# Kernel optimization log

Hardware: AMD Instinct MI355X
Metric: run time of the kernel (lower is better)

The kernel has to match this reference:

```python
import jax, jax.numpy as jnp
import numpy as np

NUM_HEADS = 8
HEAD_DIM = 64  # hidden_size 512 / 8 heads


def setup_inputs() -> dict:
    key = jax.random.key(0)
    ks = jax.random.split(key, 9)
    B, S, D, H = 64, 512, 512, 512  # batch, feat_num, input_size, hidden_size
    s = 0.02
    return {
        "x": jax.random.normal(ks[0], (B, S, D), dtype=jnp.float32),
        "wq": jax.random.normal(ks[1], (D, H), dtype=jnp.float32) * s,
        "bq": jax.random.normal(ks[2], (H,), dtype=jnp.float32) * s,
        "wk": jax.random.normal(ks[3], (D, H), dtype=jnp.float32) * s,
        "bk": jax.random.normal(ks[4], (H,), dtype=jnp.float32) * s,
        "wv": jax.random.normal(ks[5], (D, H), dtype=jnp.float32) * s,
        "bv": jax.random.normal(ks[6], (H,), dtype=jnp.float32) * s,
        "wo": jax.random.normal(ks[7], (H, D), dtype=jnp.float32) * s,
        "bo": jax.random.normal(ks[8], (D,), dtype=jnp.float32) * s,
    }


def reference(x, wq, bq, wk, bk, wv, bv, wo, bo):
    B, S, D = x.shape
    # QKV projections -> [B, heads, S, head_dim]
    def split_heads(t):
        return t.reshape(B, S, NUM_HEADS, HEAD_DIM).transpose(0, 2, 1, 3)
    q = split_heads(x @ wq + bq)
    k = split_heads(x @ wk + bk)
    v = split_heads(x @ wv + bv)
    # attention: [B, h, S, S]
    scores = jnp.einsum("bhsd,bhtd->bhst", q, k) / jnp.sqrt(
        jnp.asarray(HEAD_DIM, dtype=x.dtype)
    )
    probs = jax.nn.softmax(scores, axis=-1)  # dropout p=0 -> identity
    ctx = jnp.einsum("bhst,bhtd->bhsd", probs, v)
    ctx = ctx.transpose(0, 2, 1, 3).reshape(B, S, NUM_HEADS * HEAD_DIM)
    # output dense + residual + relu (dropout identity)
    out = jax.nn.relu(x + (ctx @ wo + bo))
    return out
```

## Files before the change

kernel.cpp:

```cpp
#include <hip/hip_runtime.h>
#include <hip/hip_bf16.h>

typedef unsigned short u16;
typedef unsigned int u32;
typedef __attribute__((ext_vector_type(8))) short short8;
typedef __attribute__((ext_vector_type(4))) float f32x4;
typedef __attribute__((ext_vector_type(4))) _Float16 f16x4;

static __device__ __forceinline__ u16 f2b(float f) {
  unsigned u = __builtin_bit_cast(unsigned, f);
  unsigned r = u + 0x7fffu + ((u >> 16) & 1u);
  return (u16)(r >> 16);
}
static __device__ __forceinline__ unsigned pk2(float a, float b) {
  return (unsigned)f2b(a) | ((unsigned)f2b(b) << 16);
}
static __device__ __forceinline__ u32 pkh(float a, float b) {
  return __builtin_bit_cast(u32, __builtin_amdgcn_cvt_pkrtz(a, b));
}

static __device__ __forceinline__ void gl_lds16(const u16* g, u16* l) {
  __builtin_amdgcn_global_load_lds(
      (const __attribute__((address_space(1))) unsigned*)g,
      (__attribute__((address_space(3))) unsigned*)l, 16, 0, 0);
}


__global__ __launch_bounds__(256) void prep(
    const float* __restrict__ wq, const float* __restrict__ wk,
    const float* __restrict__ wv, const float* __restrict__ wo,
    const float* __restrict__ x, u16* __restrict__ wqkv_t,
    u16* __restrict__ wo_t, u16* __restrict__ xb) {
  int t = blockIdx.x * 256 + threadIdx.x;
  if (t < 786432) {
    int n = t >> 9, k = t & 511;
    const float* w = (n < 512) ? wq : (n < 1024 ? wk : wv);
    wqkv_t[(size_t)n * 512 + k] = f2b(w[k * 512 + (n & 511)]);
  } else if (t < 1048576) {
    int j = t - 786432;
    int n = j >> 9, k = j & 511;
    wo_t[(size_t)n * 512 + k] = f2b(wo[k * 512 + n]);
  } else {
    size_t i = (size_t)(t - 1048576) * 4;
    float4 v = *reinterpret_cast<const float4*>(&x[i]);
    uint2 p;
    p.x = pk2(v.x, v.y);
    p.y = pk2(v.z, v.w);
    *reinterpret_cast<uint2*>(&xb[i]) = p;
  }
}

__global__ __launch_bounds__(256, 4) void gemm_qkv(
    const u16* __restrict__ xb, const u16* __restrict__ wt,
    const float* __restrict__ bq, const float* __restrict__ bk,
    const float* __restrict__ bv, u16* __restrict__ qkv) {
  __shared__ u16 As[128 * 64];
  __shared__ u16 Bs[128 * 64];
  const int tid = threadIdx.x;
  const int wave = tid >> 6, lane = tid & 63;
  const int wm = wave & 1, wn = wave >> 1;
  const int lr = lane & 15, lg = lane >> 4;
  const int n0 = blockIdx.x * 128, m0 = blockIdx.y * 128;

  const f32x4 fz = {0.f, 0.f, 0.f, 0.f};
  f32x4 acc[4][4];
#pragma unroll
  for (int i = 0; i < 4; ++i)
#pragma unroll
    for (int j = 0; j < 4; ++j) acc[i][j] = fz;

  for (int kb = 0; kb < 512; kb += 64) {
#pragma unroll
    for (int j = 0; j < 4; ++j) {
      const int cb = (wave * 4 + j) * 64;
      const int c = cb + lane;
      const int r = c >> 3;
      const int cg = (c & 7) ^ (r & 7);
      gl_lds16(&xb[(size_t)(m0 + r) * 512 + kb + (cg << 3)], &As[cb * 8]);
      gl_lds16(&wt[(size_t)(n0 + r) * 512 + kb + (cg << 3)], &Bs[cb * 8]);
    }
    __syncthreads();
#pragma unroll
    for (int ks = 0; ks < 2; ++ks) {
      short8 af[4], bb[4];
#pragma unroll
      for (int i = 0; i < 4; ++i)
        af[i] = *reinterpret_cast<const short8*>(
            &As[(wm * 64 + i * 16 + lr) * 64 +
                (((ks * 4 + lg) ^ (lr & 7)) << 3)]);
#pragma unroll
      for (int j = 0; j < 4; ++j)
        bb[j] = *reinterpret_cast<const short8*>(
            &Bs[(wn * 64 + j * 16 + lr) * 64 +
                (((ks * 4 + lg) ^ (lr & 7)) << 3)]);
#pragma unroll
      for (int i = 0; i < 4; ++i)
#pragma unroll
        for (int j = 0; j < 4; ++j)
          acc[i][j] = __builtin_amdgcn_mfma_f32_16x16x32_bf16(
              af[i], bb[j], acc[i][j], 0, 0, 0);
    }
    __syncthreads();
  }
#pragma unroll
  for (int i = 0; i < 4; ++i) {
    const int row0 = m0 + wm * 64 + i * 16 + lg * 4;
#pragma unroll
    for (int j = 0; j < 4; ++j) {
      const int col = n0 + wn * 64 + j * 16 + lr;
      const float bias =
          (col < 512) ? bq[col] : (col < 1024 ? bk[col - 512] : bv[col - 1024]);
#pragma unroll
      for (int r = 0; r < 4; ++r) {
        float v = acc[i][j][r] + bias;
        u16 ov;
        if (col < 512)
          ov = f2b(v * 0.125f);
        else if (col < 1024)
          ov = f2b(v);
        else
          ov = __builtin_bit_cast(u16, (_Float16)v);
        qkv[(size_t)(row0 + r) * 1536 + col] = ov;
      }
    }
  }
}

__global__ __launch_bounds__(256, 3) void attn(const u16* __restrict__ qkv,
                                               u16* __restrict__ ctx) {
  __shared__ u16 QOs[128 * 66];
  __shared__ u16 Ks[2][64 * 64];
  __shared__ u16 VsT[2][64 * 70];

  const int tid = threadIdx.x;
  const int wave = tid >> 6, lane = tid & 63;
  const int lr = lane & 15, lg = lane >> 4;
  const int bx = blockIdx.x;
  const int q0 = (bx & 3) * 128;
  const int h = (bx >> 2) & 7;
  const int b = bx >> 5;
  const size_t rowbase = (size_t)b * 512;

#pragma unroll
  for (int j = 0; j < 4; ++j) {
    const int cb = (wave * 4 + j) * 64, c = cb + lane;
    const int r = c >> 3, cg = (c & 7) ^ (r & 7);
    gl_lds16(&qkv[(rowbase + q0 + r) * 1536 + h * 64 + (cg << 3)],
             &QOs[cb * 8]);
  }
#pragma unroll
  for (int j = 0; j < 2; ++j) {
    const int cb = (wave * 2 + j) * 64, c = cb + lane;
    const int r = c >> 3, cg = (c & 7) ^ (r & 7);
    gl_lds16(&qkv[(rowbase + r) * 1536 + 512 + h * 64 + (cg << 3)],
             &Ks[0][cb * 8]);
  }
  uint4 vreg[2];
#pragma unroll
  for (int i = 0; i < 2; ++i) {
    int idx = tid + i * 256, r = idx >> 3, cg = idx & 7;
    vreg[i] = *reinterpret_cast<const uint4*>(
        &qkv[(rowbase + r) * 1536 + 1024 + h * 64 + cg * 8]);
  }
#pragma unroll
  for (int i = 0; i < 2; ++i) {
    int idx = tid + i * 256, r = idx >> 3, cg = idx & 7;
    const u16* pv = reinterpret_cast<const u16*>(&vreg[i]);
#pragma unroll
    for (int jj = 0; jj < 8; ++jj) VsT[0][(cg * 8 + jj) * 70 + r] = pv[jj];
  }
  __syncthreads();

  short8 aq[2][2];
#pragma unroll
  for (int g = 0; g < 2; ++g)
#pragma unroll
    for (int ks = 0; ks < 2; ++ks)
      aq[g][ks] = *reinterpret_cast<const short8*>(
          &QOs[(wave * 32 + g * 16 + lr) * 64 +
               (((ks * 4 + lg) ^ (lr & 7)) << 3)]);

  const f32x4 fz = {0.f, 0.f, 0.f, 0.f};
  f32x4 oacc[2][4];
#pragma unroll
  for (int g = 0; g < 2; ++g)
#pragma unroll
    for (int dt = 0; dt < 4; ++dt) oacc[g][dt] = fz;
  float lsum[2] = {0.f, 0.f};

  for (int tt = 0; tt < 8; ++tt) {
    const int buf = tt & 1;
    if (tt < 7) {
#pragma unroll
      for (int j = 0; j < 2; ++j) {
        const int cb = (wave * 2 + j) * 64, c = cb + lane;
        const int r = c >> 3, cg = (c & 7) ^ (r & 7);
        gl_lds16(&qkv[(rowbase + (tt + 1) * 64 + r) * 1536 + 512 + h * 64 +
                      (cg << 3)],
                 &Ks[buf ^ 1][cb * 8]);
      }
#pragma unroll
      for (int i = 0; i < 2; ++i) {
        int idx = tid + i * 256, r = idx >> 3, cg = idx & 7;
        vreg[i] = *reinterpret_cast<const uint4*>(
            &qkv[(rowbase + (tt + 1) * 64 + r) * 1536 + 1024 + h * 64 + cg * 8]);
      }
    }

    f32x4 st[2][4];
#pragma unroll
    for (int g = 0; g < 2; ++g)
#pragma unroll
      for (int mt = 0; mt < 4; ++mt) st[g][mt] = fz;
#pragma unroll
    for (int mt = 0; mt < 4; ++mt) {
      short8 k0 = *reinterpret_cast<const short8*>(
          &Ks[buf][(mt * 16 + lr) * 64 + ((lg ^ (lr & 7)) << 3)]);
      short8 k1 = *reinterpret_cast<const short8*>(
          &Ks[buf][(mt * 16 + lr) * 64 + (((4 + lg) ^ (lr & 7)) << 3)]);
#pragma unroll
      for (int g = 0; g < 2; ++g) {
        st[g][mt] = __builtin_amdgcn_mfma_f32_16x16x32_bf16(k0, aq[g][0],
                                                            st[g][mt], 0, 0, 0);
        st[g][mt] = __builtin_amdgcn_mfma_f32_16x16x32_bf16(k1, aq[g][1],
                                                            st[g][mt], 0, 0, 0);
      }
    }

    f16x4 pfrag[2][4];
#pragma unroll
    for (int g = 0; g < 2; ++g)
#pragma unroll
      for (int mt = 0; mt < 4; ++mt) {
        float e0 = __expf(st[g][mt][0]), e1 = __expf(st[g][mt][1]);
        float e2 = __expf(st[g][mt][2]), e3 = __expf(st[g][mt][3]);
        lsum[g] += (e0 + e1) + (e2 + e3);
        uint2 uu;
        uu.x = pkh(e0, e1);
        uu.y = pkh(e2, e3);
        pfrag[g][mt] = __builtin_bit_cast(f16x4, uu);
      }

#pragma unroll
    for (int dt = 0; dt < 4; ++dt) {
#pragma unroll
      for (int tw = 0; tw < 4; ++tw) {
        const int a0 = (dt * 16 + lr) * 70 + tw * 16 + lg * 4;
        uint2 uu;
        uu.x = *reinterpret_cast<const u32*>(&VsT[buf][a0]);
        uu.y = *reinterpret_cast<const u32*>(&VsT[buf][a0 + 2]);
        f16x4 vf = __builtin_bit_cast(f16x4, uu);
#pragma unroll
        for (int g = 0; g < 2; ++g)
          oacc[g][dt] = __builtin_amdgcn_mfma_f32_16x16x16f16(
              vf, pfrag[g][tw], oacc[g][dt], 0, 0, 0);
      }
    }

    if (tt < 7) {
#pragma unroll
      for (int i = 0; i < 2; ++i) {
        int idx = tid + i * 256, r = idx >> 3, cg = idx & 7;
        const u16* pv = reinterpret_cast<const u16*>(&vreg[i]);
#pragma unroll
        for (int jj = 0; jj < 8; ++jj)
          VsT[buf ^ 1][(cg * 8 + jj) * 70 + r] = pv[jj];
      }
    }
    __syncthreads();
  }

#pragma unroll
  for (int g = 0; g < 2; ++g) {
    float s = lsum[g];
    s += __shfl_xor(s, 16);
    s += __shfl_xor(s, 32);
    lsum[g] = 1.0f / s;
  }
#pragma unroll
  for (int g = 0; g < 2; ++g)
#pragma unroll
    for (int dt = 0; dt < 4; ++dt) {
      f32x4 o = oacc[g][dt];
      const float li = lsum[g];
      const int base = (wave * 32 + g * 16 + lr) * 66 + dt * 16 + lg * 4;
      *reinterpret_cast<u32*>(&QOs[base]) = pk2(o[0] * li, o[1] * li);
      *reinterpret_cast<u32*>(&QOs[base + 2]) = pk2(o[2] * li, o[3] * li);
    }
  __syncthreads();
  const size_t coff = (rowbase + q0) * 512 + h * 64;
#pragma unroll
  for (int i = 0; i < 4; ++i) {
    int idx = tid + i * 256, r = idx >> 3, cg = idx & 7;
    const u16* src = &QOs[r * 66 + cg * 8];
    uint4 w;
    w.x = *reinterpret_cast<const u32*>(&src[0]);
    w.y = *reinterpret_cast<const u32*>(&src[2]);
    w.z = *reinterpret_cast<const u32*>(&src[4]);
    w.w = *reinterpret_cast<const u32*>(&src[6]);
    *reinterpret_cast<uint4*>(&ctx[coff + (size_t)r * 512 + cg * 8]) = w;
  }
}

__global__ __launch_bounds__(256, 4) void gemm_out(
    const u16* __restrict__ ctx, const u16* __restrict__ wot,
    const float* __restrict__ x, const float* __restrict__ bo,
    float* __restrict__ out) {
  __shared__ u16 As[128 * 64];
  __shared__ u16 Bs[128 * 64];
  const int tid = threadIdx.x;
  const int wave = tid >> 6, lane = tid & 63;
  const int wm = wave & 1, wn = wave >> 1;
  const int lr = lane & 15, lg = lane >> 4;
  const int n0 = blockIdx.x * 128, m0 = blockIdx.y * 128;

  const f32x4 fz = {0.f, 0.f, 0.f, 0.f};
  f32x4 acc[4][4];
#pragma unroll
  for (int i = 0; i < 4; ++i)
#pragma unroll
    for (int j = 0; j < 4; ++j) acc[i][j] = fz;

  for (int kb = 0; kb < 512; kb += 64) {
#pragma unroll
    for (int j = 0; j < 4; ++j) {
      const int cb = (wave * 4 + j) * 64;
      const int c = cb + lane;
      const int r = c >> 3;
      const int cg = (c & 7) ^ (r & 7);
      gl_lds16(&ctx[(size_t)(m0 + r) * 512 + kb + (cg << 3)], &As[cb * 8]);
      gl_lds16(&wot[(size_t)(n0 + r) * 512 + kb + (cg << 3)], &Bs[cb * 8]);
    }
    __syncthreads();
#pragma unroll
    for (int ks = 0; ks < 2; ++ks) {
      short8 af[4], bb[4];
#pragma unroll
      for (int i = 0; i < 4; ++i)
        af[i] = *reinterpret_cast<const short8*>(
            &As[(wm * 64 + i * 16 + lr) * 64 +
                (((ks * 4 + lg) ^ (lr & 7)) << 3)]);
#pragma unroll
      for (int j = 0; j < 4; ++j)
        bb[j] = *reinterpret_cast<const short8*>(
            &Bs[(wn * 64 + j * 16 + lr) * 64 +
                (((ks * 4 + lg) ^ (lr & 7)) << 3)]);
#pragma unroll
      for (int i = 0; i < 4; ++i)
#pragma unroll
        for (int j = 0; j < 4; ++j)
          acc[i][j] = __builtin_amdgcn_mfma_f32_16x16x32_bf16(
              af[i], bb[j], acc[i][j], 0, 0, 0);
    }
    __syncthreads();
  }
#pragma unroll
  for (int i = 0; i < 4; ++i) {
#pragma unroll
    for (int j = 0; j < 4; ++j) {
      const int col = n0 + wn * 64 + j * 16 + lr;
#pragma unroll
      for (int r = 0; r < 4; ++r) {
        const int row = m0 + wm * 64 + i * 16 + lg * 4 + r;
        float v = acc[i][j][r] + bo[col] + x[(size_t)row * 512 + col];
        out[(size_t)row * 512 + col] = fmaxf(v, 0.0f);
      }
    }
  }
}

extern "C" void kernel_launch(void* const* d_in, const int* in_sizes, int n_in,
                              void* d_out, int out_size, void* d_ws,
                              size_t ws_size, hipStream_t stream) {
  const float* x = (const float*)d_in[0];
  const float* wq = (const float*)d_in[1];
  const float* bq = (const float*)d_in[2];
  const float* wk = (const float*)d_in[3];
  const float* bk = (const float*)d_in[4];
  const float* wv = (const float*)d_in[5];
  const float* bv = (const float*)d_in[6];
  const float* wo = (const float*)d_in[7];
  const float* bo = (const float*)d_in[8];
  float* out = (float*)d_out;

  char* ws = (char*)d_ws;
  u16* qkv = (u16*)ws;
  u16* ctx = (u16*)(ws + 100663296);
  u16* xb = ctx;
  u16* wqkv_t = (u16*)(ws + 134217728);
  u16* wo_t = (u16*)(ws + 135790592);

  hipLaunchKernelGGL(prep, dim3(20480), dim3(256), 0, stream, wq, wk, wv, wo,
                     x, wqkv_t, wo_t, xb);
  hipLaunchKernelGGL(gemm_qkv, dim3(12, 256), dim3(256), 0, stream, xb, wqkv_t,
                     bq, bk, bv, qkv);
  hipLaunchKernelGGL(attn, dim3(2048), dim3(256), 0, stream, qkv, ctx);
  hipLaunchKernelGGL(gemm_out, dim3(4, 256), dim3(256), 0, stream, ctx, wo_t,
                     x, bo, out);
}
```

Baseline: 307.3 us.

## Remap block indices per XCD, write ctx in place, read bf16 residual

Block indices in the QKV GEMM, attention and output GEMM are remapped so consecutive blocks on the same XCD share rows and heads, aiming for better L2 reuse. Attention writes its context output into the Q slot of the qkv buffer, and the output GEMM reads it with a 1536 stride, removing the separate ctx buffer. The residual is read from the bf16 copy of x instead of fp32 to halve those bytes. This adds rounding error to the residual path.

```diff
diff --git a/kernel.cpp b/kernel.cpp
--- a/kernel.cpp
+++ b/kernel.cpp
@@ -11,6 +11,9 @@
   unsigned u = __builtin_bit_cast(unsigned, f);
   unsigned r = u + 0x7fffu + ((u >> 16) & 1u);
   return (u16)(r >> 16);
+}
+static __device__ __forceinline__ float b2f(u16 v) {
+  return __builtin_bit_cast(float, (u32)v << 16);
 }
 static __device__ __forceinline__ unsigned pk2(float a, float b) {
   return (unsigned)f2b(a) | ((unsigned)f2b(b) << 16);
@@ -60,7 +63,10 @@
   const int wave = tid >> 6, lane = tid & 63;
   const int wm = wave & 1, wn = wave >> 1;
   const int lr = lane & 15, lg = lane >> 4;
-  const int n0 = blockIdx.x * 128, m0 = blockIdx.y * 128;
+  const int id = blockIdx.x;
+  const int xcd = id & 7, s = id >> 3;
+  const int n0 = (s % 12) * 128;
+  const int m0 = ((s / 12) * 8 + xcd) * 128;
 
   const f32x4 fz = {0.f, 0.f, 0.f, 0.f};
   f32x4 acc[4][4];
@@ -126,8 +132,7 @@
   }
 }
 
-__global__ __launch_bounds__(256, 3) void attn(const u16* __restrict__ qkv,
-                                               u16* __restrict__ ctx) {
+__global__ __launch_bounds__(256, 3) void attn(u16* __restrict__ qkv) {
   __shared__ u16 QOs[128 * 66];
   __shared__ u16 Ks[2][64 * 64];
   __shared__ u16 VsT[2][64 * 70];
@@ -136,9 +141,10 @@
   const int wave = tid >> 6, lane = tid & 63;
   const int lr = lane & 15, lg = lane >> 4;
   const int bx = blockIdx.x;
-  const int q0 = (bx & 3) * 128;
-  const int h = (bx >> 2) & 7;
-  const int b = bx >> 5;
+  const int xcd = bx & 7, s = bx >> 3;
+  const int q0 = (s & 3) * 128;
+  const int bh = (s >> 2) * 8 + xcd;
+  const int b = bh >> 3, h = bh & 7;
   const size_t rowbase = (size_t)b * 512;
 
 #pragma unroll
@@ -272,10 +278,10 @@
 
 #pragma unroll
   for (int g = 0; g < 2; ++g) {
-    float s = lsum[g];
-    s += __shfl_xor(s, 16);
-    s += __shfl_xor(s, 32);
-    lsum[g] = 1.0f / s;
+    float s2 = lsum[g];
+    s2 += __shfl_xor(s2, 16);
+    s2 += __shfl_xor(s2, 32);
+    lsum[g] = 1.0f / s2;
   }
 #pragma unroll
   for (int g = 0; g < 2; ++g)
@@ -288,7 +294,6 @@
       *reinterpret_cast<u32*>(&QOs[base + 2]) = pk2(o[2] * li, o[3] * li);
     }
   __syncthreads();
-  const size_t coff = (rowbase + q0) * 512 + h * 64;
 #pragma unroll
   for (int i = 0; i < 4; ++i) {
     int idx = tid + i * 256, r = idx >> 3, cg = idx & 7;
@@ -298,13 +303,14 @@
     w.y = *reinterpret_cast<const u32*>(&src[2]);
     w.z = *reinterpret_cast<const u32*>(&src[4]);
     w.w = *reinterpret_cast<const u32*>(&src[6]);
-    *reinterpret_cast<uint4*>(&ctx[coff + (size_t)r * 512 + cg * 8]) = w;
+    *reinterpret_cast<uint4*>(
+        &qkv[(rowbase + q0 + r) * 1536 + h * 64 + cg * 8]) = w;
   }
 }
 
 __global__ __launch_bounds__(256, 4) void gemm_out(
-    const u16* __restrict__ ctx, const u16* __restrict__ wot,
-    const float* __restrict__ x, const float* __restrict__ bo,
+    const u16* __restrict__ ctxq, const u16* __restrict__ wot,
+    const u16* __restrict__ xb, const float* __restrict__ bo,
     float* __restrict__ out) {
   __shared__ u16 As[128 * 64];
   __shared__ u16 Bs[128 * 64];
@@ -312,7 +318,10 @@
   const int wave = tid >> 6, lane = tid & 63;
   const int wm = wave & 1, wn = wave >> 1;
   const int lr = lane & 15, lg = lane >> 4;
-  const int n0 = blockIdx.x * 128, m0 = blockIdx.y * 128;
+  const int id = blockIdx.x;
+  const int xcd = id & 7, s = id >> 3;
+  const int n0 = (s & 3) * 128;
+  const int m0 = ((s >> 2) * 8 + xcd) * 128;
 
   const f32x4 fz = {0.f, 0.f, 0.f, 0.f};
   f32x4 acc[4][4];
@@ -328,7 +337,7 @@
       const int c = cb + lane;
       const int r = c >> 3;
       const int cg = (c & 7) ^ (r & 7);
-      gl_lds16(&ctx[(size_t)(m0 + r) * 512 + kb + (cg << 3)], &As[cb * 8]);
+      gl_lds16(&ctxq[(size_t)(m0 + r) * 1536 + kb + (cg << 3)], &As[cb * 8]);
       gl_lds16(&wot[(size_t)(n0 + r) * 512 + kb + (cg << 3)], &Bs[cb * 8]);
     }
     __syncthreads();
@@ -362,7 +371,7 @@
 #pragma unroll
       for (int r = 0; r < 4; ++r) {
         const int row = m0 + wm * 64 + i * 16 + lg * 4 + r;
-        float v = acc[i][j][r] + bo[col] + x[(size_t)row * 512 + col];
+        float v = acc[i][j][r] + bo[col] + b2f(xb[(size_t)row * 512 + col]);
         out[(size_t)row * 512 + col] = fmaxf(v, 0.0f);
       }
     }
@@ -385,16 +394,15 @@
 
   char* ws = (char*)d_ws;
   u16* qkv = (u16*)ws;
-  u16* ctx = (u16*)(ws + 100663296);
-  u16* xb = ctx;
+  u16* xb = (u16*)(ws + 100663296);
   u16* wqkv_t = (u16*)(ws + 134217728);
   u16* wo_t = (u16*)(ws + 135790592);
 
   hipLaunchKernelGGL(prep, dim3(20480), dim3(256), 0, stream, wq, wk, wv, wo,
                      x, wqkv_t, wo_t, xb);
-  hipLaunchKernelGGL(gemm_qkv, dim3(12, 256), dim3(256), 0, stream, xb, wqkv_t,
+  hipLaunchKernelGGL(gemm_qkv, dim3(3072), dim3(256), 0, stream, xb, wqkv_t,
                      bq, bk, bv, qkv);
-  hipLaunchKernelGGL(attn, dim3(2048), dim3(256), 0, stream, qkv, ctx);
-  hipLaunchKernelGGL(gemm_out, dim3(4, 256), dim3(256), 0, stream, ctx, wo_t,
-                     x, bo, out);
-}
+  hipLaunchKernelGGL(attn, dim3(2048), dim3(256), 0, stream, qkv);
+  hipLaunchKernelGGL(gemm_out, dim3(1024), dim3(256), 0, stream, qkv, wo_t,
+                     xb, bo, out);
+}
```

Result: faster. 277.9 us (-9.6%).
